# Optimization experiments

Measured on AMD Instinct MI355X. Metric: run time of the kernel, lower is better.

## Reference

```python
import jax, jax.numpy as jnp
import numpy as np
from jax import lax

D_MODEL = 96; D_STATE = 16; D_INNER = 192; DT_RANK = 6; K = 4
BSZ = 2; HH = 64; WW = 64


def setup_inputs() -> dict:
    key = jax.random.key(0)
    ks = jax.random.split(key, 16)
    f = lambda k, shape, s=0.02: (jax.random.normal(k, shape) * s).astype(jnp.float32)
    P = DT_RANK + 2 * D_STATE
    return {
        "x": jax.random.normal(ks[0], (BSZ, HH, WW, D_MODEL), jnp.float32),
        "W_in": f(ks[1], (2 * D_INNER, D_MODEL)),
        "b_in": jnp.zeros((2 * D_INNER,), jnp.float32),
        "conv_w": f(ks[2], (D_INNER, 1, 3, 3)),
        "conv_b": jnp.zeros((D_INNER,), jnp.float32),
        "W_xp": f(ks[3], (K * P, K * D_INNER)),
        "b_xp": jnp.zeros((K * P,), jnp.float32),
        "W_dt": f(ks[4], (K * D_INNER, K * DT_RANK)),
        "b_dt": f(ks[5], (K * D_INNER,), 0.1),
        "A_log": jax.random.normal(ks[6], (K * D_INNER, D_STATE), jnp.float32),
        "D_skip": jnp.ones((K * D_INNER,), jnp.float32),
        "dt_bias": jax.random.normal(ks[7], (K * D_INNER,), jnp.float32),
        "W_out": f(ks[8], (D_MODEL, D_INNER)),
        "b_out": jnp.zeros((D_MODEL,), jnp.float32),
        "gamma": jnp.ones((D_INNER,), jnp.float32),
        "beta": jnp.zeros((D_INNER,), jnp.float32),
    }


def cross_scan(x):
    # x: (B, D, H, W) -> (B, 4, D, L); dirs: row-major, col-major, and their reverses
    B, D, H, W = x.shape
    L = H * W
    x0 = x.reshape(B, D, L)
    x1 = jnp.swapaxes(x, 2, 3).reshape(B, D, L)
    return jnp.stack([x0, x1, x0[..., ::-1], x1[..., ::-1]], axis=1)


def cross_merge(ys):
    # ys: (B, 4, D, H, W) -> (B, D, L); inverse of cross_scan, summed
    B, Kk, D, H, W = ys.shape
    L = H * W
    yf = ys.reshape(B, Kk, D, L)
    y02 = yf[:, 0] + yf[:, 2, :, ::-1]
    y13 = yf[:, 1] + yf[:, 3, :, ::-1]
    y13 = jnp.swapaxes(y13.reshape(B, D, W, H), 2, 3).reshape(B, D, L)
    return y02 + y13


def selective_scan(u, dt, A, Bm, Cm, D_skip, dt_bias):
    # u, dt: (B,K,Dv,L); A: (K,Dv,N); Bm, Cm: (B,K,N,L); D_skip, dt_bias: (K,Dv)
    # NOTE: torch code repeats Bm/Cm across Dv; we broadcast instead (same math).
    dt = jax.nn.softplus(dt + dt_bias[None, :, :, None])
    dt_l = jnp.moveaxis(dt, -1, 0)   # (L,B,K,Dv)
    u_l = jnp.moveaxis(u, -1, 0)     # (L,B,K,Dv)
    B_l = jnp.moveaxis(Bm, -1, 0)    # (L,B,K,N)
    C_l = jnp.moveaxis(Cm, -1, 0)    # (L,B,K,N)

    def step(h, inp):
        dt_t, u_t, b_t, c_t = inp
        dA = jnp.exp(dt_t[..., None] * A[None])                 # (B,K,Dv,N)
        dBu = (dt_t * u_t)[..., None] * b_t[:, :, None, :]      # (B,K,Dv,N)
        h = dA * h + dBu
        y = jnp.einsum('bkdn,bkn->bkd', h, c_t)
        return h, y

    h0 = jnp.zeros(u.shape[:3] + (A.shape[-1],), u.dtype)
    _, ys = lax.scan(step, h0, (dt_l, u_l, B_l, C_l))
    ys = jnp.moveaxis(ys, 0, -1)  # (B,K,Dv,L)
    return ys + u * D_skip[None, :, :, None]


def reference(x, W_in, b_in, conv_w, conv_b, W_xp, b_xp, W_dt, b_dt,
              A_log, D_skip, dt_bias, W_out, b_out, gamma, beta):
    B, H, W, _ = x.shape
    L = H * W
    xz = x @ W_in.T + b_in
    xx, z = jnp.split(xz, 2, axis=-1)
    z = jax.nn.silu(z)
    xc = jnp.transpose(xx, (0, 3, 1, 2))  # (B, D, H, W)
    xc = lax.conv_general_dilated(xc, conv_w, (1, 1), 'SAME',
                                  feature_group_count=D_INNER,
                                  dimension_numbers=('NCHW', 'OIHW', 'NCHW'))
    xc = jax.nn.silu(xc + conv_b[None, :, None, None])

    xs = cross_scan(xc)                      # (B, K, D, L)
    xs_flat = xs.reshape(B, K * D_INNER, L)

    x_dbl = jnp.einsum('bcl,pc->bpl', xs_flat, W_xp) + b_xp[None, :, None]
    x_dbl = x_dbl.reshape(B, K, DT_RANK + 2 * D_STATE, L)
    dts, Bm, Cm = jnp.split(x_dbl, [DT_RANK, DT_RANK + D_STATE], axis=2)
    dts = dts.reshape(B, K * DT_RANK, L)
    dts = jnp.einsum('brl,dr->bdl', dts, W_dt) + b_dt[None, :, None]

    A = -jnp.exp(A_log).reshape(K, D_INNER, D_STATE)
    u = xs_flat.reshape(B, K, D_INNER, L)
    dt = dts.reshape(B, K, D_INNER, L)
    ys = selective_scan(u, dt, A, Bm, Cm,
                        D_skip.reshape(K, D_INNER), dt_bias.reshape(K, D_INNER))

    y = cross_merge(ys.reshape(B, K, D_INNER, H, W))  # (B, D, L)
    y = jnp.transpose(y.reshape(B, D_INNER, H, W), (0, 2, 3, 1))

    mu = jnp.mean(y, axis=-1, keepdims=True)
    var = jnp.mean(jnp.square(y - mu), axis=-1, keepdims=True)
    y = (y - mu) * lax.rsqrt(var + 1e-5) * gamma + beta
    y = y * z
    return y @ W_out.T + b_out
```

## Files before the change

kernel.cpp:

```cpp
#include <hip/hip_runtime.h>
#include <cstdint>
#include <cstddef>


#define CHUNK 16
#define NCK   256

#if __has_builtin(__builtin_amdgcn_exp2f)
#define EXP2(x) __builtin_amdgcn_exp2f(x)
#else
#define EXP2(x) exp2f(x)
#endif
#define LOG2E 1.44269504088896340736f
#define KSTRIDE 196608

typedef __attribute__((ext_vector_type(8))) short short8;
typedef __attribute__((ext_vector_type(8))) unsigned short ushort8;
typedef __attribute__((ext_vector_type(4))) float f32x4;

__device__ __forceinline__ float siluf(float x){ return x * (1.f/(1.f+__expf(-x))); }
__device__ __forceinline__ float softplusf(float v){
  return (v > 20.f) ? v : log1pf(__expf(v));
}
__device__ __forceinline__ unsigned short f2b(float f){
  uint32_t u = __float_as_uint(f);
  uint32_t r = (u + 0x7fffu + ((u>>16)&1u)) >> 16;
  return (unsigned short)r;
}

template<int KD, int STRA, int STRB>
__device__ __forceinline__ void micro_mm_T(const float (&As)[64][STRA], const float (&BsT)[KD][STRB],
                                           int tx, int ty, float (&acc)[4][4])
{
#pragma unroll 2
  for (int k4 = 0; k4 < KD/4; k4++){
    float a[4][4];
#pragma unroll
    for (int i = 0; i < 4; i++){
      float4 t = *(const float4*)&As[ty*4+i][k4*4];
      a[i][0]=t.x; a[i][1]=t.y; a[i][2]=t.z; a[i][3]=t.w;
    }
#pragma unroll
    for (int e = 0; e < 4; e++){
      float4 b = *(const float4*)&BsT[k4*4+e][tx*4];
#pragma unroll
      for (int i = 0; i < 4; i++){
        acc[i][0] = fmaf(a[i][e], b.x, acc[i][0]);
        acc[i][1] = fmaf(a[i][e], b.y, acc[i][1]);
        acc[i][2] = fmaf(a[i][e], b.z, acc[i][2]);
        acc[i][3] = fmaf(a[i][e], b.w, acc[i][3]);
      }
    }
  }
}

__global__ __launch_bounds__(256) void k_cast_w(
    const float* __restrict__ Wxp, unsigned short* __restrict__ Wf)
{
  int tid = blockIdx.x*256 + threadIdx.x;
  if (tid >= 18432) return;
  int lane = tid & 63; int rest = tid >> 6;
  int pt = rest % 6; rest /= 6;
  int k32 = rest & 3; rest >>= 2;
  int kc = rest % 6; int ph = rest / 6;
  int n = lane & 15, q = lane >> 4;
  int p = ph*96 + pt*16 + n;
  int kbase = kc*128 + k32*32 + q*8;
  unsigned short v[8];
#pragma unroll
  for (int j = 0; j < 8; j++)
    v[j] = (p < 152) ? f2b(Wxp[(size_t)p*768 + kbase + j]) : (unsigned short)0;
  *(ushort8*)(Wf + (size_t)tid*8) = *(ushort8*)v;
}

__global__ __launch_bounds__(256) void k_gemm_in(
    const float* __restrict__ x, const float* __restrict__ W,
    const float* __restrict__ bias, float* __restrict__ xx, float* __restrict__ zs)
{
  __shared__ float As[64][100];
  __shared__ float BsT[96][68];
  const int m0 = blockIdx.x*64, n0 = blockIdx.y*64;
  const int tid = threadIdx.x;
#pragma unroll
  for (int i = 0; i < 6; i++){
    int idx = tid + i*256;
    { int r = idx/24, c4 = idx%24;
      *(float4*)&As[r][c4*4] = *(const float4*)(x + (size_t)(m0+r)*96 + c4*4); }
    { int r = idx & 63, c4 = idx >> 6;
      float4 wv = *(const float4*)(W + (size_t)(n0+r)*96 + c4*4);
      BsT[c4*4+0][r]=wv.x; BsT[c4*4+1][r]=wv.y; BsT[c4*4+2][r]=wv.z; BsT[c4*4+3][r]=wv.w; }
  }
  __syncthreads();
  const int tx = tid & 15, ty = tid >> 4;
  float acc[4][4] = {};
  micro_mm_T<96,100,68>(As, BsT, tx, ty, acc);
#pragma unroll
  for (int i = 0; i < 4; i++){
    int m = m0 + ty*4 + i;
#pragma unroll
    for (int j = 0; j < 4; j++){
      int n = n0 + tx*4 + j;
      float v = acc[i][j] + bias[n];
      if (n < 192) xx[(size_t)m*192 + n] = v;
      else         zs[(size_t)m*192 + (n-192)] = siluf(v);
    }
  }
}

__global__ __launch_bounds__(256) void k_conv(
    const float* __restrict__ xx, const float* __restrict__ cw, const float* __restrict__ cb,
    float* __restrict__ xc,
    unsigned short* __restrict__ xcb, unsigned short* __restrict__ xcTb)
{
  int gid = blockIdx.x*256 + threadIdx.x;
  int c = gid % 192;
  int l = (gid/192) & 4095;
  int b = gid / (192*4096);
  int h = l >> 6, w = l & 63;
  float s = 0.f;
#pragma unroll
  for (int kh = 0; kh < 3; kh++){
    int h2 = h + kh - 1;
    if ((unsigned)h2 >= 64u) continue;
#pragma unroll
    for (int kw = 0; kw < 3; kw++){
      int w2 = w + kw - 1;
      if ((unsigned)w2 >= 64u) continue;
      s += xx[((size_t)b*4096 + h2*64 + w2)*192 + c] * cw[c*9 + kh*3 + kw];
    }
  }
  s = siluf(s + cb[c]);
  unsigned short sb = f2b(s);
  size_t i0 = ((size_t)b*4096 + l)*192 + c;
  xc[i0] = s; xcb[i0] = sb;
  int tl = (l & 63)*64 + (l >> 6);
  xcTb[((size_t)b*4096 + tl)*192 + c] = sb;
}

__global__ __launch_bounds__(256) void k_gemm_xdbl(
    const unsigned short* __restrict__ xcb, const unsigned short* __restrict__ xcTb,
    const unsigned short* __restrict__ Wf, const float* __restrict__ bxp,
    float* __restrict__ xdbl)
{
  __shared__ unsigned short Bsh[4*6*64*8];
  const int tid = threadIdx.x;
  const int lane = tid & 63, w = tid >> 6;
  const int wl = w & 1, wp = w >> 1;
  const int l0 = blockIdx.x*64, ph = blockIdx.y, b = blockIdx.z;
  const int n = lane & 15, q = lane >> 4;
  f32x4 acc[2][3] = {};
  const unsigned short* slab0 = Wf + (size_t)ph*6*12288;
  for (int kc = 0; kc < 6; kc++){
    __syncthreads();
    const ushort8* srcp = (const ushort8*)(slab0 + (size_t)kc*12288);
#pragma unroll
    for (int t = 0; t < 6; t++) ((ushort8*)Bsh)[tid + t*256] = srcp[tid + t*256];
    __syncthreads();
#pragma unroll
    for (int k32 = 0; k32 < 4; k32++){
      int kk = kc*128 + k32*32;
      int dir = kk/192; int ch = kk%192 + q*8;
      const unsigned short* sp = (dir & 1) ? xcTb : xcb;
      bool rev = (dir >= 2);
      short8 a[2];
#pragma unroll
      for (int mt = 0; mt < 2; mt++){
        int ls = l0 + wl*32 + mt*16 + n;
        int row = rev ? 4095 - ls : ls;
        a[mt] = *(const short8*)(sp + ((size_t)b*4096 + row)*192 + ch);
      }
#pragma unroll
      for (int j = 0; j < 3; j++){
        short8 bfr = *(const short8*)&Bsh[((size_t)(k32*6 + wp*3 + j)*64 + lane)*8];
#pragma unroll
        for (int mt = 0; mt < 2; mt++)
          acc[mt][j] = __builtin_amdgcn_mfma_f32_16x16x32_bf16(a[mt], bfr, acc[mt][j], 0, 0, 0);
      }
    }
  }
#pragma unroll
  for (int mt = 0; mt < 2; mt++)
#pragma unroll
    for (int j = 0; j < 3; j++){
      int p = ph*96 + (wp*3+j)*16 + n;
      if (p < 152){
        int k = p/38, pp = p%38;
        int off = (pp < 6) ? pp : pp + 2;
        float bias = bxp[p];
#pragma unroll
        for (int reg = 0; reg < 4; reg++){
          int l = l0 + wl*32 + mt*16 + q*4 + reg;
          xdbl[(((size_t)b*4 + k)*4096 + l)*48 + off] = acc[mt][j][reg] + bias;
        }
      }
    }
}

__global__ __launch_bounds__(256) void k_scanA(
    const float* __restrict__ xc, const float* __restrict__ xdbl,
    const float* __restrict__ A_log, const float* __restrict__ Wdt,
    const float* __restrict__ bdt, const float* __restrict__ dtbias,
    float* __restrict__ dte, float* __restrict__ Pb, float* __restrict__ Sb)
{
  const int lane = threadIdx.x & 63;
  const int wid  = __builtin_amdgcn_readfirstlane(blockIdx.x*4 + (threadIdx.x >> 6));
  const int ck = wid & (NCK-1); const int g = wid / NCK;
  const int dblk = g % 3; const int bk = g / 3;
  const int k = bk & 3; const int b = bk >> 2;
  const int d = dblk*64 + lane; const int ch = k*192 + d;
  float An[16];
  {
    const float4* ap = (const float4*)(A_log + (size_t)ch*16);
#pragma unroll
    for (int i = 0; i < 4; i++){
      float4 t = ap[i];
      An[4*i+0] = -LOG2E*__expf(t.x); An[4*i+1] = -LOG2E*__expf(t.y);
      An[4*i+2] = -LOG2E*__expf(t.z); An[4*i+3] = -LOG2E*__expf(t.w);
    }
  }
  float Wr[24];
#pragma unroll
  for (int r = 0; r < 24; r++) Wr[r] = Wdt[(size_t)ch*24 + r];
  const float bsum = bdt[ch] + dtbias[ch];
  const int l0 = ck*CHUNK;
  const bool rev = (k >= 2);
  const int tr = k & 1;
  const int T0 = tr ? ((l0 & 63)*64 + (l0 >> 6)) : l0;
  const int rs = tr ? 64 : 1;
  const int row0 = rev ? 4095 - T0 : T0;
  const int rstep = (rev ? -rs : rs)*192;
  const float* up  = xc + ((size_t)b*4096 + row0)*192 + d;
  const float* xq  = xdbl + ((size_t)b*4*4096 + l0)*48;
  const float* xbc = xq + (size_t)k*KSTRIDE;
  float* dtw = dte + (((size_t)b*4 + k)*4096 + l0)*192 + d;
  float h[16];
#pragma unroll
  for (int n = 0; n < 16; n++) h[n] = 0.f;
  float sdt = 0.f;
#pragma unroll 2
  for (int t = 0; t < CHUNK; t++){
    float u  = up[0];
    float4 B0 = *(const float4*)(xbc + 8);
    float4 B1 = *(const float4*)(xbc + 12);
    float4 B2 = *(const float4*)(xbc + 16);
    float4 B3 = *(const float4*)(xbc + 20);
    float Bv[16] = {B0.x,B0.y,B0.z,B0.w, B1.x,B1.y,B1.z,B1.w,
                    B2.x,B2.y,B2.z,B2.w, B3.x,B3.y,B3.z,B3.w};
    float v0 = bsum, v1 = 0.f;
#pragma unroll
    for (int kp = 0; kp < 4; kp++){
      const float* qp = xq + (size_t)kp*KSTRIDE;
      float4 a  = *(const float4*)(qp);
      float2 b2 = *(const float2*)(qp + 4);
      v0 = fmaf(Wr[kp*6+0], a.x, v0);  v1 = fmaf(Wr[kp*6+1], a.y, v1);
      v0 = fmaf(Wr[kp*6+2], a.z, v0);  v1 = fmaf(Wr[kp*6+3], a.w, v1);
      v0 = fmaf(Wr[kp*6+4], b2.x, v0); v1 = fmaf(Wr[kp*6+5], b2.y, v1);
    }
    float dt = softplusf(v0 + v1);
    dtw[0] = dt;
    float dtu = dt*u;
    sdt += dt;
#pragma unroll
    for (int n = 0; n < 16; n++){
      float dA = EXP2(dt*An[n]);
      h[n] = fmaf(dA, h[n], dtu*Bv[n]);
    }
    xq += 48; xbc += 48; up += rstep; dtw += 192;
  }
  size_t base = ((size_t)wid*16)*64 + lane;
#pragma unroll
  for (int n = 0; n < 16; n++){
    Pb[base + n*64] = EXP2(An[n]*sdt);
    Sb[base + n*64] = h[n];
  }
}

__global__ __launch_bounds__(256) void k_scanB(
    const float* __restrict__ Pb, const float* __restrict__ Sb, float* __restrict__ H0)
{
  int tid = blockIdx.x*256 + threadIdx.x;
  int lane = tid & 63; int n = (tid >> 6) & 15; int g = tid >> 10;
  float h = 0.f;
#pragma unroll 4
  for (int ck = 0; ck < NCK; ck++){
    size_t idx = (((size_t)(g*NCK + ck)*16) + n)*64 + lane;
    H0[idx] = h;
    h = fmaf(Pb[idx], h, Sb[idx]);
  }
}

__global__ __launch_bounds__(256) void k_scanC(
    const float* __restrict__ xc, const float* __restrict__ xdbl,
    const float* __restrict__ A_log, const float* __restrict__ dte,
    const float* __restrict__ Dskip,
    const float* __restrict__ H0, float* __restrict__ ys)
{
  const int lane = threadIdx.x & 63;
  const int wid  = __builtin_amdgcn_readfirstlane(blockIdx.x*4 + (threadIdx.x >> 6));
  const int ck = wid & (NCK-1); const int g = wid / NCK;
  const int dblk = g % 3; const int bk = g / 3;
  const int k = bk & 3; const int b = bk >> 2;
  const int d = dblk*64 + lane; const int ch = k*192 + d;
  float An[16];
  {
    const float4* ap = (const float4*)(A_log + (size_t)ch*16);
#pragma unroll
    for (int i = 0; i < 4; i++){
      float4 t = ap[i];
      An[4*i+0] = -LOG2E*__expf(t.x); An[4*i+1] = -LOG2E*__expf(t.y);
      An[4*i+2] = -LOG2E*__expf(t.z); An[4*i+3] = -LOG2E*__expf(t.w);
    }
  }
  const float Dv = Dskip[ch];
  const int l0 = ck*CHUNK;
  const bool rev = (k >= 2);
  const int tr = k & 1;
  const int T0 = tr ? ((l0 & 63)*64 + (l0 >> 6)) : l0;
  const int rs = tr ? 64 : 1;
  const int row0 = rev ? 4095 - T0 : T0;
  const int rstep = (rev ? -rs : rs)*192;
  const float* up  = xc + ((size_t)b*4096 + row0)*192 + d;
  const float* xbc = xdbl + (((size_t)b*4 + k)*4096 + l0)*48;
  const float* dtp = dte + (((size_t)b*4 + k)*4096 + l0)*192 + d;
  float* ysp = ys + ((size_t)(k*2 + b))*4096*192 + (size_t)row0*192 + d;
  float h[16];
  size_t base = ((size_t)wid*16)*64 + lane;
#pragma unroll
  for (int n = 0; n < 16; n++) h[n] = H0[base + n*64];
#pragma unroll 2
  for (int t = 0; t < CHUNK; t++){
    float u  = up[0];
    float dt = dtp[0];
    float4 B0 = *(const float4*)(xbc + 8);
    float4 B1 = *(const float4*)(xbc + 12);
    float4 B2 = *(const float4*)(xbc + 16);
    float4 B3 = *(const float4*)(xbc + 20);
    float4 C0 = *(const float4*)(xbc + 24);
    float4 C1 = *(const float4*)(xbc + 28);
    float4 C2 = *(const float4*)(xbc + 32);
    float4 C3 = *(const float4*)(xbc + 36);
    float Bv[16] = {B0.x,B0.y,B0.z,B0.w, B1.x,B1.y,B1.z,B1.w,
                    B2.x,B2.y,B2.z,B2.w, B3.x,B3.y,B3.z,B3.w};
    float Cv[16] = {C0.x,C0.y,C0.z,C0.w, C1.x,C1.y,C1.z,C1.w,
                    C2.x,C2.y,C2.z,C2.w, C3.x,C3.y,C3.z,C3.w};
    float dtu = dt*u;
    float y0 = u*Dv, y1 = 0.f;
#pragma unroll
    for (int n = 0; n < 16; n += 2){
      float dA0 = EXP2(dt*An[n]);
      float dA1 = EXP2(dt*An[n+1]);
      h[n]   = fmaf(dA0, h[n],   dtu*Bv[n]);
      h[n+1] = fmaf(dA1, h[n+1], dtu*Bv[n+1]);
      y0 = fmaf(h[n],   Cv[n],   y0);
      y1 = fmaf(h[n+1], Cv[n+1], y1);
    }
    ysp[0] = y0 + y1;
    xbc += 48; dtp += 192; up += rstep; ysp += rstep;
  }
}

__global__ __launch_bounds__(256) void k_ln(
    const float* __restrict__ ys, const float* __restrict__ zs,
    const float* __restrict__ gamma, const float* __restrict__ beta,
    float* __restrict__ yln)
{
  int row = blockIdx.x*4 + (threadIdx.x >> 6);
  int lane = threadIdx.x & 63;
  int b = row >> 12; int l = row & 4095;
  float v[3];
#pragma unroll
  for (int j = 0; j < 3; j++){
    int c = lane + j*64;
    float s = 0.f;
#pragma unroll
    for (int k = 0; k < 4; k++) s += ys[(((size_t)k*2 + b)*4096 + l)*192 + c];
    v[j] = s;
  }
  float tot = v[0] + v[1] + v[2];
#pragma unroll
  for (int o = 1; o < 64; o <<= 1) tot += __shfl_xor(tot, o);
  float mean = tot * (1.f/192.f);
  float d0 = v[0]-mean, d1 = v[1]-mean, d2 = v[2]-mean;
  float vs = d0*d0 + d1*d1 + d2*d2;
#pragma unroll
  for (int o = 1; o < 64; o <<= 1) vs += __shfl_xor(vs, o);
  float rstd = rsqrtf(vs*(1.f/192.f) + 1e-5f);
  float nd[3] = {d0, d1, d2};
#pragma unroll
  for (int j = 0; j < 3; j++){
    int c = lane + j*64;
    float val = nd[j]*rstd*gamma[c] + beta[c];
    val *= zs[(size_t)row*192 + c];
    yln[(size_t)row*192 + c] = val;
  }
}

__global__ __launch_bounds__(256) void k_gemm_out(
    const float* __restrict__ yln, const float* __restrict__ Wout,
    const float* __restrict__ bout, float* __restrict__ out)
{
  __shared__ float As[64][100];
  __shared__ float BsT[96][68];
  const int m0 = blockIdx.x*64, n0 = blockIdx.y*64;
  const int tid = threadIdx.x;
  const int tx = tid & 15, ty = tid >> 4;
  float acc[4][4] = {};
  for (int kc = 0; kc < 2; kc++){
    __syncthreads();
#pragma unroll
    for (int i = 0; i < 6; i++){
      int idx = tid + i*256;
      { int r = idx/24, c4 = idx%24;
        *(float4*)&As[r][c4*4] = *(const float4*)(yln + (size_t)(m0+r)*192 + kc*96 + c4*4); }
      { int r = idx & 63, c4 = idx >> 6;
        int nn = n0 + r;
        float4 wv = make_float4(0.f,0.f,0.f,0.f);
        if (nn < 96) wv = *(const float4*)(Wout + (size_t)nn*192 + kc*96 + c4*4);
        BsT[c4*4+0][r]=wv.x; BsT[c4*4+1][r]=wv.y; BsT[c4*4+2][r]=wv.z; BsT[c4*4+3][r]=wv.w; }
    }
    __syncthreads();
    micro_mm_T<96,100,68>(As, BsT, tx, ty, acc);
  }
#pragma unroll
  for (int i = 0; i < 4; i++){
    int m = m0 + ty*4 + i;
#pragma unroll
    for (int j = 0; j < 4; j++){
      int n = n0 + tx*4 + j;
      if (n < 96) out[(size_t)m*96 + n] = acc[i][j] + bout[n];
    }
  }
}

extern "C" void kernel_launch(void* const* d_in, const int* in_sizes, int n_in,
                              void* d_out, int out_size, void* d_ws, size_t ws_size,
                              hipStream_t stream)
{
  const float* x      = (const float*)d_in[0];
  const float* W_in   = (const float*)d_in[1];
  const float* b_in   = (const float*)d_in[2];
  const float* conv_w = (const float*)d_in[3];
  const float* conv_b = (const float*)d_in[4];
  const float* W_xp   = (const float*)d_in[5];
  const float* b_xp   = (const float*)d_in[6];
  const float* W_dt   = (const float*)d_in[7];
  const float* b_dt   = (const float*)d_in[8];
  const float* A_log  = (const float*)d_in[9];
  const float* D_skip = (const float*)d_in[10];
  const float* dt_bias= (const float*)d_in[11];
  const float* W_out  = (const float*)d_in[12];
  const float* b_out  = (const float*)d_in[13];
  const float* gamma  = (const float*)d_in[14];
  const float* beta   = (const float*)d_in[15];
  float* out = (float*)d_out;

  float* ws   = (float*)d_ws;
  float* xx   = ws;
  float* zs   = ws + 1572864;
  float* xc   = ws + 3145728;
  float* xdbl = ws + 4718592;
  float* ysb  = ws + 6291456;
  float* yln  = ws + 12582912;
  float* dte  = ws + 14155776;
  float* Pb   = ws + 20447232;
  float* Sb   = ws + 26738688;
  float* H0   = ws + 33030144;
  unsigned short* xcb  = (unsigned short*)(ws + 39321600);
  unsigned short* xcTb = xcb + 1572864;
  unsigned short* Wf   = (unsigned short*)(ws + 40894464);

  k_cast_w   <<<72,             256, 0, stream>>>(W_xp, Wf);
  k_gemm_in  <<<dim3(128, 6),   256, 0, stream>>>(x, W_in, b_in, xx, zs);
  k_conv     <<<6144,           256, 0, stream>>>(xx, conv_w, conv_b, xc, xcb, xcTb);
  k_gemm_xdbl<<<dim3(64, 2, 2), 256, 0, stream>>>(xcb, xcTb, Wf, b_xp, xdbl);
  k_scanA    <<<1536,           256, 0, stream>>>(xc, xdbl, A_log, W_dt, b_dt, dt_bias, dte, Pb, Sb);
  k_scanB    <<<96,             256, 0, stream>>>(Pb, Sb, H0);
  k_scanC    <<<1536,           256, 0, stream>>>(xc, xdbl, A_log, dte, D_skip, H0, ysb);
  k_ln       <<<2048,           256, 0, stream>>>(ysb, zs, gamma, beta, yln);
  k_gemm_out <<<dim3(128, 2),   256, 0, stream>>>(yln, W_out, b_out, out);
}
```

Baseline: 257.2 us.

## Pack dt projections contiguously, faster softplus, smaller scanB blocks, deeper unroll

The xdbl GEMM now also writes the 24 dt-rank values for all four directions into a compact per-position buffer. scanA can then fetch them with six contiguous float4 loads instead of four strided gathers across directions, and it sums them with four accumulators. Softplus now uses exp2/log2 intrinsics instead of log1pf, which costs some precision for small values. scanB moves to 64-thread blocks so more blocks are spread across CUs, and the scan loops are unrolled further.

Result: faster. 227.0 us (-11.7%).

```diff
diff --git a/kernel.cpp b/kernel.cpp
--- a/kernel.cpp
+++ b/kernel.cpp
@@ -12,15 +12,17 @@
 #define EXP2(x) exp2f(x)
 #endif
 #define LOG2E 1.44269504088896340736f
-#define KSTRIDE 196608
+#define LN2   0.69314718055994530942f
 
 typedef __attribute__((ext_vector_type(8))) short short8;
 typedef __attribute__((ext_vector_type(8))) unsigned short ushort8;
 typedef __attribute__((ext_vector_type(4))) float f32x4;
 
 __device__ __forceinline__ float siluf(float x){ return x * (1.f/(1.f+__expf(-x))); }
-__device__ __forceinline__ float softplusf(float v){
-  return (v > 20.f) ? v : log1pf(__expf(v));
+__device__ __forceinline__ float softplus_fast(float v){
+  float e  = EXP2(v*LOG2E);
+  float sp = LN2*__log2f(1.f + e);
+  return (v > 20.f) ? v : sp;
 }
 __device__ __forceinline__ unsigned short f2b(float f){
   uint32_t u = __float_as_uint(f);
@@ -140,7 +142,7 @@
 __global__ __launch_bounds__(256) void k_gemm_xdbl(
     const unsigned short* __restrict__ xcb, const unsigned short* __restrict__ xcTb,
     const unsigned short* __restrict__ Wf, const float* __restrict__ bxp,
-    float* __restrict__ xdbl)
+    float* __restrict__ xdbl, float* __restrict__ dts_c)
 {
   __shared__ unsigned short Bsh[4*6*64*8];
   const int tid = threadIdx.x;
@@ -190,7 +192,9 @@
 #pragma unroll
         for (int reg = 0; reg < 4; reg++){
           int l = l0 + wl*32 + mt*16 + q*4 + reg;
-          xdbl[(((size_t)b*4 + k)*4096 + l)*48 + off] = acc[mt][j][reg] + bias;
+          float val = acc[mt][j][reg] + bias;
+          xdbl[(((size_t)b*4 + k)*4096 + l)*48 + off] = val;
+          if (pp < 6) dts_c[((size_t)b*4096 + l)*24 + k*6 + pp] = val;
         }
       }
     }
@@ -198,6 +202,7 @@
 
 __global__ __launch_bounds__(256) void k_scanA(
     const float* __restrict__ xc, const float* __restrict__ xdbl,
+    const float* __restrict__ dts_c,
     const float* __restrict__ A_log, const float* __restrict__ Wdt,
     const float* __restrict__ bdt, const float* __restrict__ dtbias,
     float* __restrict__ dte, float* __restrict__ Pb, float* __restrict__ Sb)
@@ -230,14 +235,14 @@
   const int row0 = rev ? 4095 - T0 : T0;
   const int rstep = (rev ? -rs : rs)*192;
   const float* up  = xc + ((size_t)b*4096 + row0)*192 + d;
-  const float* xq  = xdbl + ((size_t)b*4*4096 + l0)*48;
-  const float* xbc = xq + (size_t)k*KSTRIDE;
+  const float* qc  = dts_c + ((size_t)b*4096 + l0)*24;
+  const float* xbc = xdbl + (((size_t)b*4 + k)*4096 + l0)*48;
   float* dtw = dte + (((size_t)b*4 + k)*4096 + l0)*192 + d;
   float h[16];
 #pragma unroll
   for (int n = 0; n < 16; n++) h[n] = 0.f;
   float sdt = 0.f;
-#pragma unroll 2
+#pragma unroll 4
   for (int t = 0; t < CHUNK; t++){
     float u  = up[0];
     float4 B0 = *(const float4*)(xbc + 8);
@@ -246,17 +251,24 @@
     float4 B3 = *(const float4*)(xbc + 20);
     float Bv[16] = {B0.x,B0.y,B0.z,B0.w, B1.x,B1.y,B1.z,B1.w,
                     B2.x,B2.y,B2.z,B2.w, B3.x,B3.y,B3.z,B3.w};
-    float v0 = bsum, v1 = 0.f;
-#pragma unroll
-    for (int kp = 0; kp < 4; kp++){
-      const float* qp = xq + (size_t)kp*KSTRIDE;
-      float4 a  = *(const float4*)(qp);
-      float2 b2 = *(const float2*)(qp + 4);
-      v0 = fmaf(Wr[kp*6+0], a.x, v0);  v1 = fmaf(Wr[kp*6+1], a.y, v1);
-      v0 = fmaf(Wr[kp*6+2], a.z, v0);  v1 = fmaf(Wr[kp*6+3], a.w, v1);
-      v0 = fmaf(Wr[kp*6+4], b2.x, v0); v1 = fmaf(Wr[kp*6+5], b2.y, v1);
-    }
-    float dt = softplusf(v0 + v1);
+    float4 q0 = *(const float4*)(qc);
+    float4 q1 = *(const float4*)(qc + 4);
+    float4 q2 = *(const float4*)(qc + 8);
+    float4 q3 = *(const float4*)(qc + 12);
+    float4 q4 = *(const float4*)(qc + 16);
+    float4 q5 = *(const float4*)(qc + 20);
+    float qv[24] = {q0.x,q0.y,q0.z,q0.w, q1.x,q1.y,q1.z,q1.w,
+                    q2.x,q2.y,q2.z,q2.w, q3.x,q3.y,q3.z,q3.w,
+                    q4.x,q4.y,q4.z,q4.w, q5.x,q5.y,q5.z,q5.w};
+    float v0 = bsum, v1 = 0.f, v2 = 0.f, v3 = 0.f;
+#pragma unroll
+    for (int r = 0; r < 24; r += 4){
+      v0 = fmaf(Wr[r+0], qv[r+0], v0);
+      v1 = fmaf(Wr[r+1], qv[r+1], v1);
+      v2 = fmaf(Wr[r+2], qv[r+2], v2);
+      v3 = fmaf(Wr[r+3], qv[r+3], v3);
+    }
+    float dt = softplus_fast((v0+v1) + (v2+v3));
     dtw[0] = dt;
     float dtu = dt*u;
     sdt += dt;
@@ -265,7 +277,7 @@
       float dA = EXP2(dt*An[n]);
       h[n] = fmaf(dA, h[n], dtu*Bv[n]);
     }
-    xq += 48; xbc += 48; up += rstep; dtw += 192;
+    qc += 24; xbc += 48; up += rstep; dtw += 192;
   }
   size_t base = ((size_t)wid*16)*64 + lane;
 #pragma unroll
@@ -275,13 +287,13 @@
   }
 }
 
-__global__ __launch_bounds__(256) void k_scanB(
+__global__ __launch_bounds__(64) void k_scanB(
     const float* __restrict__ Pb, const float* __restrict__ Sb, float* __restrict__ H0)
 {
-  int tid = blockIdx.x*256 + threadIdx.x;
+  int tid = blockIdx.x*64 + threadIdx.x;
   int lane = tid & 63; int n = (tid >> 6) & 15; int g = tid >> 10;
   float h = 0.f;
-#pragma unroll 4
+#pragma unroll 8
   for (int ck = 0; ck < NCK; ck++){
     size_t idx = (((size_t)(g*NCK + ck)*16) + n)*64 + lane;
     H0[idx] = h;
@@ -327,7 +339,7 @@
   size_t base = ((size_t)wid*16)*64 + lane;
 #pragma unroll
   for (int n = 0; n < 16; n++) h[n] = H0[base + n*64];
-#pragma unroll 2
+#pragma unroll 4
   for (int t = 0; t < CHUNK; t++){
     float u  = up[0];
     float dt = dtp[0];
@@ -454,27 +466,28 @@
   const float* beta   = (const float*)d_in[15];
   float* out = (float*)d_out;
 
-  float* ws   = (float*)d_ws;
-  float* xx   = ws;
-  float* zs   = ws + 1572864;
-  float* xc   = ws + 3145728;
-  float* xdbl = ws + 4718592;
-  float* ysb  = ws + 6291456;
-  float* yln  = ws + 12582912;
-  float* dte  = ws + 14155776;
-  float* Pb   = ws + 20447232;
-  float* Sb   = ws + 26738688;
-  float* H0   = ws + 33030144;
-  unsigned short* xcb  = (unsigned short*)(ws + 39321600);
+  float* ws    = (float*)d_ws;
+  float* xx    = ws;
+  float* zs    = ws + 1572864;
+  float* xc    = ws + 3145728;
+  float* xdbl  = ws + 4718592;
+  float* ysb   = ws + 6291456;
+  float* yln   = ws + 12582912;
+  float* dte   = ws + 14155776;
+  float* Pb    = ws + 20447232;
+  float* Sb    = ws + 26738688;
+  float* H0    = ws + 33030144;
+  float* dts_c = ws + 39321600;
+  unsigned short* xcb  = (unsigned short*)(ws + 39518208);
   unsigned short* xcTb = xcb + 1572864;
-  unsigned short* Wf   = (unsigned short*)(ws + 40894464);
+  unsigned short* Wf   = (unsigned short*)(ws + 41091072);
 
   k_cast_w   <<<72,             256, 0, stream>>>(W_xp, Wf);
   k_gemm_in  <<<dim3(128, 6),   256, 0, stream>>>(x, W_in, b_in, xx, zs);
   k_conv     <<<6144,           256, 0, stream>>>(xx, conv_w, conv_b, xc, xcb, xcTb);
-  k_gemm_xdbl<<<dim3(64, 2, 2), 256, 0, stream>>>(xcb, xcTb, Wf, b_xp, xdbl);
-  k_scanA    <<<1536,           256, 0, stream>>>(xc, xdbl, A_log, W_dt, b_dt, dt_bias, dte, Pb, Sb);
-  k_scanB    <<<96,             256, 0, stream>>>(Pb, Sb, H0);
+  k_gemm_xdbl<<<dim3(64, 2, 2), 256, 0, stream>>>(xcb, xcTb, Wf, b_xp, xdbl, dts_c);
+  k_scanA    <<<1536,           256, 0, stream>>>(xc, xdbl, dts_c, A_log, W_dt, b_dt, dt_bias, dte, Pb, Sb);
+  k_scanB    <<<384,            64,  0, stream>>>(Pb, Sb, H0);
   k_scanC    <<<1536,           256, 0, stream>>>(xc, xdbl, A_log, dte, D_skip, H0, ysb);
   k_ln       <<<2048,           256, 0, stream>>>(ysb, zs, gamma, beta, yln);
   k_gemm_out <<<dim3(128, 2),   256, 0, stream>>>(yln, W_out, b_out, out);
```
